# Kernel tuning notes

Hardware: AMD Instinct MI355X
Metric: run time of the kernel (lower is better)

Reference implementation:

```python
import jax, jax.numpy as jnp
import numpy as np

BATCH, SEQ, D_IN = 4, 2048, 1024
STATE, D_OUT, KX = 1024, 1024, 10


def setup_inputs() -> dict:
    key = jax.random.key(0)
    k0, k1, k2, k3, k4, k5 = jax.random.split(key, 6)
    inputs = jax.random.normal(k0, (BATCH, SEQ, D_IN), jnp.float32)
    h0 = jax.random.normal(k1, (STATE,), jnp.float32)
    A = jax.random.normal(k2, (STATE,), jnp.float32)
    A = A / jnp.max(jnp.abs(A))  # matches init_A / max|init_A|
    B = jax.random.normal(k3, (D_IN, STATE), jnp.float32) / D_IN
    C = jax.random.normal(k4, (STATE, D_OUT), jnp.float32) / STATE
    M = jax.random.normal(k5, (D_IN, D_OUT, KX), jnp.float32) / D_OUT
    return {"inputs": inputs, "h0": h0, "A": A, "B": B, "C": C, "M": M}


def compute_ar_x_preds(w, x):
    # w: (d_out, d_in, k); x: (b, l, d_in)
    d_out, d_in, k = w.shape
    b, l, _ = x.shape
    o = jnp.einsum('oik,bli->bklo', w, x)  # (b, k, l, d_out)
    shifts = jnp.arange(k)
    # roll slice i forward by i along the length axis
    o = jax.vmap(lambda oi, s: jnp.roll(oi, s, axis=1), in_axes=(1, 0), out_axes=1)(o, shifts)
    # triu mask: keep position t in slice i only if t >= i (causal AR)
    m = (jnp.arange(l)[None, :] >= shifts[:, None]).astype(o.dtype)  # (k, l)
    return jnp.sum(o * m[None, :, :, None], axis=1)  # (b, l, d_out)


def reference(inputs, h0, A, B, C, M):
    bsz = inputs.shape[0]
    h_init = jnp.broadcast_to(h0, (bsz, h0.shape[0]))  # h0.expand(bsz, state_dim)
    u_seq = jnp.swapaxes(inputs, 0, 1)  # (l, b, d_in)

    def step(h, u):
        h_new = A * h + u @ B  # diagonal recurrence
        return h_new, h_new

    _, hs = jax.lax.scan(step, h_init, u_seq)  # (l, b, state)
    all_h_t = jnp.swapaxes(hs, 0, 1)  # (b, l, state)
    lds_out = all_h_t @ C  # (b, l, d_out)
    ar = compute_ar_x_preds(M, inputs)
    return lds_out + ar
```

## Files before the change

kernel.cpp:

```cpp
#include <hip/hip_runtime.h>
#include <stdint.h>

typedef unsigned short u16;
typedef __attribute__((ext_vector_type(4))) float f32x4;
typedef __attribute__((ext_vector_type(8))) short s16x8;

#define BATCH 4
#define SEQ   2048
#define DIM   1024
#define KX    10
#define PAD   16
#define SEQP  (SEQ+PAD)

__device__ __forceinline__ u16 f2b(float f) {
    union { float f; uint32_t u; } v; v.f = f;
    uint32_t u = v.u + 0x7fffu + ((v.u >> 16) & 1u);
    return (u16)(u >> 16);
}
__device__ __forceinline__ float b2f(u16 h) {
    union { uint32_t u; float f; } v; v.u = ((uint32_t)h) << 16;
    return v.f;
}

__device__ __forceinline__ void llds16(const u16* g, u16* l) {
    __builtin_amdgcn_global_load_lds(
        (const __attribute__((address_space(1))) uint32_t*)g,
        (__attribute__((address_space(3))) uint32_t*)l, 16, 0, 0);
}

#define PREP_X_END  8256
#define PREP_C_END  10304
#define PREP_M_END  14400

__global__ __launch_bounds__(256) void k_prep(
    const float* __restrict__ x, const float* __restrict__ B,
    const float* __restrict__ C, const float* __restrict__ M,
    u16* __restrict__ Xpad, u16* __restrict__ Btr, u16* __restrict__ Wall)
{
    __shared__ float tile[32][33];
    const int bid = blockIdx.x, tid = threadIdx.x;

    if (bid < PREP_X_END) {
        int idx = bid * 256 + tid;
        long e = (long)idx * 4;
        int i = (int)(e & 1023);
        int row = (int)(e >> 10);
        int t = row % SEQP;
        int b = row / SEQP;
        ushort4 o;
        if (t < PAD) {
            o.x = 0; o.y = 0; o.z = 0; o.w = 0;
        } else {
            const float4 v = *(const float4*)(x + (((long)(b * SEQ + (t - PAD)) << 10) + i));
            o.x = f2b(v.x); o.y = f2b(v.y); o.z = f2b(v.z); o.w = f2b(v.w);
        }
        *(ushort4*)(Xpad + ((long)row << 10) + i) = o;
    } else if (bid < PREP_C_END) {
        const int tb = bid - PREP_X_END;
        const float* in = (tb < 1024) ? B : C;
        u16* out = (tb < 1024) ? Btr : Wall;
        int lb = tb & 1023;
        int bx = lb & 31, by = lb >> 5;
        int tx = tid & 31, ty = tid >> 5;
#pragma unroll
        for (int j = 0; j < 4; j++)
            tile[ty + j * 8][tx] = in[(long)(by * 32 + ty + j * 8) * 1024 + bx * 32 + tx];
        __syncthreads();
#pragma unroll
        for (int j = 0; j < 4; j++)
            out[(long)(bx * 32 + ty + j * 8) * 1024 + by * 32 + tx] = f2b(tile[tx][ty + j * 8]);
    } else {
        int idx = (bid - PREP_C_END) * 256 + tid;
        int o = idx >> 10, i = idx & 1023;
        const float* src = M + (long)idx * KX;
#pragma unroll
        for (int k = 0; k < KX; k++)
            Wall[((long)(k + 1) << 20) + ((long)o << 10) + i] = f2b(src[k]);
    }
}


__global__ void k_scan1(const u16* __restrict__ U, const float* __restrict__ A,
                        float* __restrict__ F) {
    int s = blockIdx.x * 256 + threadIdx.x;
    int bc = blockIdx.y;
    int b = bc >> 4, c = bc & 15;
    float a = A[s];
    const u16* u = U + (((long)(b * SEQ + c * 128)) << 10) + s;
    float f = 0.f;
#pragma unroll 8
    for (int j = 0; j < 128; j++) f = fmaf(a, f, b2f(u[(long)j << 10]));
    F[((long)bc << 10) + s] = f;
}

__global__ void k_scan2(const float* __restrict__ F, const float* __restrict__ A,
                        const float* __restrict__ h0, float* __restrict__ Carry) {
    int idx = blockIdx.x * 256 + threadIdx.x;
    int b = idx >> 10, s = idx & 1023;
    float a = A[s];
    float a128 = a;
#pragma unroll
    for (int q = 0; q < 7; q++) a128 *= a128;
    float carry = h0[s];
#pragma unroll
    for (int c = 0; c < 16; c++) {
        long off = ((long)(b * 16 + c) << 10) + s;
        Carry[off] = carry;
        carry = fmaf(a128, carry, F[off]);
    }
}

__global__ void k_scan3(u16* __restrict__ U, const float* __restrict__ A,
                        const float* __restrict__ Carry) {
    int s = blockIdx.x * 256 + threadIdx.x;
    int bc = blockIdx.y;
    int b = bc >> 4, c = bc & 15;
    float a = A[s];
    long base = (((long)(b * SEQ + c * 128)) << 10) + s;
    float h = Carry[((long)bc << 10) + s];
#pragma unroll 8
    for (int j = 0; j < 128; j++) {
        h = fmaf(a, h, b2f(U[base + ((long)j << 10)]));
        U[base + ((long)j << 10)] = f2b(h);
    }
}

__global__ __launch_bounds__(256) void k_gemm(
    void* __restrict__ outv, const u16* __restrict__ Xpad,
    const u16* __restrict__ Hbf, const u16* __restrict__ W,
    int ngroups, int use_h, int bf16_out)
{
    __shared__ u16 Asl[160 * 64];
    __shared__ u16 Wb2[2][128 * 64];

    const int tid  = threadIdx.x;
    const int wave = tid >> 6, lane = tid & 63;
    const int wm = wave >> 1, wn = wave & 1;
    const int quad = lane >> 4, l15 = lane & 15, l7 = lane & 7;

    const int col0 = blockIdx.x * 128;
    const int row0 = blockIdx.y * 128;
    const int bb = row0 >> 11;
    const long Xrow0 = (long)bb * SEQP + PAD + (row0 & (SEQ - 1));
    const long XslabBase = (Xrow0 - 16) << 10;
    const int lastg = ngroups - 1;

    f32x4 acc[4][4];
#pragma unroll
    for (int i = 0; i < 4; i++)
#pragma unroll
        for (int j = 0; j < 4; j++)
            acc[i][j] = (f32x4){0.f, 0.f, 0.f, 0.f};

    for (int k0 = 0; k0 < 1024; k0 += 64) {
#pragma unroll
        for (int q = 0; q < 5; q++) {
            int u = wave * 320 + q * 64 + lane;
            int row = u >> 3;
            int kc = (u & 7) ^ (row & 7);
            llds16(Xpad + XslabBase + ((long)row << 10) + k0 + kc * 8,
                   &Asl[(wave * 320 + q * 64) * 8]);
        }
        {
            int wsel = use_h ? 1 : 0;
            const u16* Wg = W + ((long)wsel << 20) + ((long)col0 << 10);
#pragma unroll
            for (int q = 0; q < 4; q++) {
                int u = wave * 256 + q * 64 + lane;
                int row = u >> 3;
                int kc = (u & 7) ^ (row & 7);
                llds16(Wg + ((long)row << 10) + k0 + kc * 8,
                       &Wb2[0][(wave * 256 + q * 64) * 8]);
            }
        }
        __syncthreads();

        for (int g = 0; g < ngroups; g++) {
            const bool isH = use_h && (g == lastg);
            if (isH) {
                const u16* Hb = Hbf + ((long)row0 << 10);
#pragma unroll
                for (int q = 0; q < 4; q++) {
                    int u = wave * 256 + q * 64 + lane;
                    int row = u >> 3;
                    int kc = (u & 7) ^ (row & 7);
                    llds16(Hb + ((long)row << 10) + k0 + kc * 8,
                           &Asl[(wave * 256 + q * 64) * 8]);
                }
                __syncthreads();
            }
            if (g < lastg) {
                int gn = g + 1;
                int wsel = use_h ? ((gn == lastg) ? 0 : gn + 1) : gn;
                const u16* Wg = W + ((long)wsel << 20) + ((long)col0 << 10);
                u16* dst = Wb2[gn & 1];
#pragma unroll
                for (int q = 0; q < 4; q++) {
                    int u = wave * 256 + q * 64 + lane;
                    int row = u >> 3;
                    int kc = (u & 7) ^ (row & 7);
                    llds16(Wg + ((long)row << 10) + k0 + kc * 8,
                           &dst[(wave * 256 + q * 64) * 8]);
                }
            }

            const int rbase = isH ? 0 : (16 - g);
            const int r7 = (l15 + rbase) & 7;
            const u16* Wrd = Wb2[g & 1];

            s16x8 af[4][2], bfr[4][2];
#pragma unroll
            for (int mi = 0; mi < 4; mi++) {
                int arow = rbase + wm * 64 + mi * 16 + l15;
#pragma unroll
                for (int kk = 0; kk < 2; kk++) {
                    int kca = ((kk * 4 + quad) ^ r7) << 3;
                    int kcb = ((kk * 4 + quad) ^ l7) << 3;
                    af[mi][kk]  = *(const s16x8*)&Asl[arow * 64 + kca];
                    bfr[mi][kk] = *(const s16x8*)&Wrd[(wn * 64 + mi * 16 + l15) * 64 + kcb];
                }
            }
#pragma unroll
            for (int mi = 0; mi < 4; mi++)
#pragma unroll
                for (int ni = 0; ni < 4; ni++) {
                    acc[mi][ni] = __builtin_amdgcn_mfma_f32_16x16x32_bf16(
                        af[mi][0], bfr[ni][0], acc[mi][ni], 0, 0, 0);
                    acc[mi][ni] = __builtin_amdgcn_mfma_f32_16x16x32_bf16(
                        af[mi][1], bfr[ni][1], acc[mi][ni], 0, 0, 0);
                }
            __syncthreads();
        }
    }

#pragma unroll
    for (int mi = 0; mi < 4; mi++) {
        int r = row0 + wm * 64 + mi * 16 + quad * 4;
#pragma unroll
        for (int ni = 0; ni < 4; ni++) {
            int c = col0 + wn * 64 + ni * 16 + l15;
            f32x4 v = acc[mi][ni];
            if (bf16_out) {
                u16* ob = (u16*)outv;
#pragma unroll
                for (int reg = 0; reg < 4; reg++)
                    ob[((long)(r + reg) << 10) + c] = f2b(v[reg]);
            } else {
                float* of = (float*)outv;
#pragma unroll
                for (int reg = 0; reg < 4; reg++)
                    of[((long)(r + reg) << 10) + c] = v[reg];
            }
        }
    }
}


extern "C" void kernel_launch(void* const* d_in, const int* in_sizes, int n_in,
                              void* d_out, int out_size, void* d_ws, size_t ws_size,
                              hipStream_t stream) {
    const float* x  = (const float*)d_in[0];
    const float* h0 = (const float*)d_in[1];
    const float* A  = (const float*)d_in[2];
    const float* B  = (const float*)d_in[3];
    const float* C  = (const float*)d_in[4];
    const float* M  = (const float*)d_in[5];
    float* out = (float*)d_out;

    char* ws = (char*)d_ws;
    u16*   Xpad  = (u16*)  (ws);
    u16*   Wall  = (u16*)  (ws + 16908288);
    u16*   Btr   = (u16*)  (ws + 39976960);
    u16*   Ubf   = (u16*)  (ws + 42074112);
    float* F     = (float*)(ws + 58851328);
    float* Carry = (float*)(ws + 59113472);

    k_prep<<<dim3(PREP_M_END), dim3(256), 0, stream>>>(x, B, C, M, Xpad, Btr, Wall);

    k_gemm<<<dim3(8, 64), dim3(256), 0, stream>>>(Ubf, Xpad, Ubf, Btr, 1, 0, 1);

    k_scan1<<<dim3(4, 64), dim3(256), 0, stream>>>(Ubf, A, F);
    k_scan2<<<dim3(16), dim3(256), 0, stream>>>(F, A, h0, Carry);
    k_scan3<<<dim3(4, 64), dim3(256), 0, stream>>>(Ubf, A, Carry);

    k_gemm<<<dim3(8, 64), dim3(256), 0, stream>>>(out, Xpad, Ubf, Wall, 11, 1, 0);
}
```

Before: 337.0 us.

## Load GEMM weight fragments directly into registers and template the kernel

The weight tile no longer goes through LDS. Each wave loads its B fragments straight from global memory into registers, double-buffered across the groups. The H slab gets its own LDS buffer loaded up front, which removes the per-group __syncthreads barriers and the mid-loop H reload. The kernel is templated on group count and flags so the group loop fully unrolls, it asks for 2 blocks per CU via launch bounds, and the grid is flattened to 1D. The cost is uncoalesced 16-byte global loads of W per lane and higher register pressure.

```diff
diff --git a/kernel.cpp b/kernel.cpp
--- a/kernel.cpp
+++ b/kernel.cpp
@@ -125,25 +125,25 @@
     }
 }
 
-__global__ __launch_bounds__(256) void k_gemm(
+template<int NG, int USE_H, int BF16_OUT>
+__global__ __launch_bounds__(256, 2) void k_gemm(
     void* __restrict__ outv, const u16* __restrict__ Xpad,
-    const u16* __restrict__ Hbf, const u16* __restrict__ W,
-    int ngroups, int use_h, int bf16_out)
+    const u16* __restrict__ Hbf, const u16* __restrict__ W)
 {
     __shared__ u16 Asl[160 * 64];
-    __shared__ u16 Wb2[2][128 * 64];
+    __shared__ u16 Hsl[(USE_H ? 128 : 1) * 64];
 
     const int tid  = threadIdx.x;
     const int wave = tid >> 6, lane = tid & 63;
     const int wm = wave >> 1, wn = wave & 1;
-    const int quad = lane >> 4, l15 = lane & 15, l7 = lane & 7;
-
-    const int col0 = blockIdx.x * 128;
-    const int row0 = blockIdx.y * 128;
+    const int quad = lane >> 4, l15 = lane & 15;
+
+    const int bid  = blockIdx.x;
+    const int col0 = (bid & 7) * 128;
+    const int row0 = (bid >> 3) * 128;
     const int bb = row0 >> 11;
     const long Xrow0 = (long)bb * SEQP + PAD + (row0 & (SEQ - 1));
     const long XslabBase = (Xrow0 - 16) << 10;
-    const int lastg = ngroups - 1;
 
     f32x4 acc[4][4];
 #pragma unroll
@@ -151,6 +151,8 @@
 #pragma unroll
         for (int j = 0; j < 4; j++)
             acc[i][j] = (f32x4){0.f, 0.f, 0.f, 0.f};
+
+    s16x8 bfrag[2][8];
 
     for (int k0 = 0; k0 < 1024; k0 += 64) {
 #pragma unroll
@@ -161,63 +163,55 @@
             llds16(Xpad + XslabBase + ((long)row << 10) + k0 + kc * 8,
                    &Asl[(wave * 320 + q * 64) * 8]);
         }
-        {
-            int wsel = use_h ? 1 : 0;
-            const u16* Wg = W + ((long)wsel << 20) + ((long)col0 << 10);
+        if (USE_H) {
+            const u16* Hb = Hbf + ((long)row0 << 10);
 #pragma unroll
             for (int q = 0; q < 4; q++) {
                 int u = wave * 256 + q * 64 + lane;
                 int row = u >> 3;
                 int kc = (u & 7) ^ (row & 7);
-                llds16(Wg + ((long)row << 10) + k0 + kc * 8,
-                       &Wb2[0][(wave * 256 + q * 64) * 8]);
-            }
+                llds16(Hb + ((long)row << 10) + k0 + kc * 8,
+                       &Hsl[(wave * 256 + q * 64) * 8]);
+            }
+        }
+        {
+            const int wsel0 = USE_H ? 1 : 0;
+            const u16* wp = W + ((long)wsel0 << 20) + ((long)(col0 + wn * 64) << 10) + k0;
+#pragma unroll
+            for (int ni = 0; ni < 4; ni++)
+#pragma unroll
+                for (int kk = 0; kk < 2; kk++)
+                    bfrag[0][ni * 2 + kk] =
+                        *(const s16x8*)(wp + ((l15 + ni * 16) << 10) + kk * 32 + quad * 8);
         }
         __syncthreads();
 
-        for (int g = 0; g < ngroups; g++) {
-            const bool isH = use_h && (g == lastg);
-            if (isH) {
-                const u16* Hb = Hbf + ((long)row0 << 10);
-#pragma unroll
-                for (int q = 0; q < 4; q++) {
-                    int u = wave * 256 + q * 64 + lane;
-                    int row = u >> 3;
-                    int kc = (u & 7) ^ (row & 7);
-                    llds16(Hb + ((long)row << 10) + k0 + kc * 8,
-                           &Asl[(wave * 256 + q * 64) * 8]);
-                }
-                __syncthreads();
-            }
-            if (g < lastg) {
-                int gn = g + 1;
-                int wsel = use_h ? ((gn == lastg) ? 0 : gn + 1) : gn;
-                const u16* Wg = W + ((long)wsel << 20) + ((long)col0 << 10);
-                u16* dst = Wb2[gn & 1];
-#pragma unroll
-                for (int q = 0; q < 4; q++) {
-                    int u = wave * 256 + q * 64 + lane;
-                    int row = u >> 3;
-                    int kc = (u & 7) ^ (row & 7);
-                    llds16(Wg + ((long)row << 10) + k0 + kc * 8,
-                           &dst[(wave * 256 + q * 64) * 8]);
-                }
-            }
-
+#pragma unroll
+        for (int g = 0; g < NG; g++) {
+            if (g + 1 < NG) {
+                const int wsel = USE_H ? ((g + 1 == NG - 1) ? 0 : g + 2) : g + 1;
+                const u16* wp = W + ((long)wsel << 20) + ((long)(col0 + wn * 64) << 10) + k0;
+#pragma unroll
+                for (int ni = 0; ni < 4; ni++)
+#pragma unroll
+                    for (int kk = 0; kk < 2; kk++)
+                        bfrag[(g + 1) & 1][ni * 2 + kk] =
+                            *(const s16x8*)(wp + ((l15 + ni * 16) << 10) + kk * 32 + quad * 8);
+            }
+
+            const bool isH = USE_H && (g == NG - 1);
+            const u16* abase = isH ? Hsl : Asl;
             const int rbase = isH ? 0 : (16 - g);
             const int r7 = (l15 + rbase) & 7;
-            const u16* Wrd = Wb2[g & 1];
-
-            s16x8 af[4][2], bfr[4][2];
+
+            s16x8 af[4][2];
 #pragma unroll
             for (int mi = 0; mi < 4; mi++) {
                 int arow = rbase + wm * 64 + mi * 16 + l15;
 #pragma unroll
                 for (int kk = 0; kk < 2; kk++) {
                     int kca = ((kk * 4 + quad) ^ r7) << 3;
-                    int kcb = ((kk * 4 + quad) ^ l7) << 3;
-                    af[mi][kk]  = *(const s16x8*)&Asl[arow * 64 + kca];
-                    bfr[mi][kk] = *(const s16x8*)&Wrd[(wn * 64 + mi * 16 + l15) * 64 + kcb];
+                    af[mi][kk] = *(const s16x8*)&abase[arow * 64 + kca];
                 }
             }
 #pragma unroll
@@ -225,12 +219,12 @@
 #pragma unroll
                 for (int ni = 0; ni < 4; ni++) {
                     acc[mi][ni] = __builtin_amdgcn_mfma_f32_16x16x32_bf16(
-                        af[mi][0], bfr[ni][0], acc[mi][ni], 0, 0, 0);
+                        af[mi][0], bfrag[g & 1][ni * 2 + 0], acc[mi][ni], 0, 0, 0);
                     acc[mi][ni] = __builtin_amdgcn_mfma_f32_16x16x32_bf16(
-                        af[mi][1], bfr[ni][1], acc[mi][ni], 0, 0, 0);
+                        af[mi][1], bfrag[g & 1][ni * 2 + 1], acc[mi][ni], 0, 0, 0);
                 }
-            __syncthreads();
-        }
+        }
+        __syncthreads();
     }
 
 #pragma unroll
@@ -240,7 +234,7 @@
         for (int ni = 0; ni < 4; ni++) {
             int c = col0 + wn * 64 + ni * 16 + l15;
             f32x4 v = acc[mi][ni];
-            if (bf16_out) {
+            if (BF16_OUT) {
                 u16* ob = (u16*)outv;
 #pragma unroll
                 for (int reg = 0; reg < 4; reg++)
@@ -277,11 +271,11 @@
 
     k_prep<<<dim3(PREP_M_END), dim3(256), 0, stream>>>(x, B, C, M, Xpad, Btr, Wall);
 
-    k_gemm<<<dim3(8, 64), dim3(256), 0, stream>>>(Ubf, Xpad, Ubf, Btr, 1, 0, 1);
+    k_gemm<1, 0, 1><<<dim3(512), dim3(256), 0, stream>>>(Ubf, Xpad, Ubf, Btr);
 
     k_scan1<<<dim3(4, 64), dim3(256), 0, stream>>>(Ubf, A, F);
     k_scan2<<<dim3(16), dim3(256), 0, stream>>>(F, A, h0, Carry);
     k_scan3<<<dim3(4, 64), dim3(256), 0, stream>>>(Ubf, A, Carry);
 
-    k_gemm<<<dim3(8, 64), dim3(256), 0, stream>>>(out, Xpad, Ubf, Wall, 11, 1, 0);
-}
+    k_gemm<11, 1, 0><<<dim3(512), dim3(256), 0, stream>>>(out, Xpad, Ubf, Wall);
+}
```

Result: slower. 510.0 us (+51.3%).

## Enlarge GEMM tiles to 256 rows, template kernel, split-K with atomics for output

Applied to the files above, without the earlier changes.

The GEMM kernel is templated on group count, H usage, output type and K-split, and compiled with unrolled group loops. Each block now runs 512 threads over a 256x128 tile, so each weight tile loaded into LDS is reused across twice as many rows. The final output GEMM splits K in two and accumulates into a zeroed output with float atomics, restoring grid parallelism after the larger tiles. This costs an extra memset, atomic traffic, nondeterministic summation order, higher LDS use per block, and shifted workspace offsets to pad the larger input slab.

```diff
diff --git a/kernel.cpp b/kernel.cpp
--- a/kernel.cpp
+++ b/kernel.cpp
@@ -125,25 +125,29 @@
     }
 }
 
-__global__ __launch_bounds__(256) void k_gemm(
+template<int NG, int USE_H, int BF16_OUT, int KSPLIT>
+__global__ __launch_bounds__(512, 4) void k_gemm(
     void* __restrict__ outv, const u16* __restrict__ Xpad,
-    const u16* __restrict__ Hbf, const u16* __restrict__ W,
-    int ngroups, int use_h, int bf16_out)
+    const u16* __restrict__ Hbf, const u16* __restrict__ W)
 {
-    __shared__ u16 Asl[160 * 64];
+    __shared__ u16 Asl[320 * 64];
     __shared__ u16 Wb2[2][128 * 64];
 
     const int tid  = threadIdx.x;
     const int wave = tid >> 6, lane = tid & 63;
     const int wm = wave >> 1, wn = wave & 1;
-    const int quad = lane >> 4, l15 = lane & 15, l7 = lane & 7;
-
-    const int col0 = blockIdx.x * 128;
-    const int row0 = blockIdx.y * 128;
+    const int quad = lane >> 4, l15 = lane & 15;
+
+    const int bid  = blockIdx.x;
+    const int col0 = (bid & 7) * 128;
+    const int row0 = ((bid >> 3) & 31) * 256;
+    const int kh   = (KSPLIT > 1) ? (bid >> 8) : 0;
+    const int kbeg = kh * (1024 / KSPLIT);
+    const int kend = kbeg + (1024 / KSPLIT);
+
     const int bb = row0 >> 11;
     const long Xrow0 = (long)bb * SEQP + PAD + (row0 & (SEQ - 1));
     const long XslabBase = (Xrow0 - 16) << 10;
-    const int lastg = ngroups - 1;
 
     f32x4 acc[4][4];
 #pragma unroll
@@ -152,7 +156,7 @@
         for (int j = 0; j < 4; j++)
             acc[i][j] = (f32x4){0.f, 0.f, 0.f, 0.f};
 
-    for (int k0 = 0; k0 < 1024; k0 += 64) {
+    for (int k0 = kbeg; k0 < kend; k0 += 64) {
 #pragma unroll
         for (int q = 0; q < 5; q++) {
             int u = wave * 320 + q * 64 + lane;
@@ -162,21 +166,22 @@
                    &Asl[(wave * 320 + q * 64) * 8]);
         }
         {
-            int wsel = use_h ? 1 : 0;
-            const u16* Wg = W + ((long)wsel << 20) + ((long)col0 << 10);
-#pragma unroll
-            for (int q = 0; q < 4; q++) {
-                int u = wave * 256 + q * 64 + lane;
+            const int wsel0 = USE_H ? 1 : 0;
+            const u16* Wg = W + ((long)wsel0 << 20) + ((long)col0 << 10);
+#pragma unroll
+            for (int q = 0; q < 2; q++) {
+                int u = wave * 128 + q * 64 + lane;
                 int row = u >> 3;
                 int kc = (u & 7) ^ (row & 7);
                 llds16(Wg + ((long)row << 10) + k0 + kc * 8,
-                       &Wb2[0][(wave * 256 + q * 64) * 8]);
+                       &Wb2[0][(wave * 128 + q * 64) * 8]);
             }
         }
         __syncthreads();
 
-        for (int g = 0; g < ngroups; g++) {
-            const bool isH = use_h && (g == lastg);
+#pragma unroll
+        for (int g = 0; g < NG; g++) {
+            const bool isH = USE_H && (g == NG - 1);
             if (isH) {
                 const u16* Hb = Hbf + ((long)row0 << 10);
 #pragma unroll
@@ -189,18 +194,17 @@
                 }
                 __syncthreads();
             }
-            if (g < lastg) {
-                int gn = g + 1;
-                int wsel = use_h ? ((gn == lastg) ? 0 : gn + 1) : gn;
+            if (g + 1 < NG) {
+                const int wsel = USE_H ? ((g + 1 == NG - 1) ? 0 : g + 2) : g + 1;
                 const u16* Wg = W + ((long)wsel << 20) + ((long)col0 << 10);
-                u16* dst = Wb2[gn & 1];
-#pragma unroll
-                for (int q = 0; q < 4; q++) {
-                    int u = wave * 256 + q * 64 + lane;
+                u16* dst = Wb2[(g + 1) & 1];
+#pragma unroll
+                for (int q = 0; q < 2; q++) {
+                    int u = wave * 128 + q * 64 + lane;
                     int row = u >> 3;
                     int kc = (u & 7) ^ (row & 7);
                     llds16(Wg + ((long)row << 10) + k0 + kc * 8,
-                           &dst[(wave * 256 + q * 64) * 8]);
+                           &dst[(wave * 128 + q * 64) * 8]);
                 }
             }
 
@@ -215,7 +219,7 @@
 #pragma unroll
                 for (int kk = 0; kk < 2; kk++) {
                     int kca = ((kk * 4 + quad) ^ r7) << 3;
-                    int kcb = ((kk * 4 + quad) ^ l7) << 3;
+                    int kcb = ((kk * 4 + quad) ^ (l15 & 7)) << 3;
                     af[mi][kk]  = *(const s16x8*)&Asl[arow * 64 + kca];
                     bfr[mi][kk] = *(const s16x8*)&Wrd[(wn * 64 + mi * 16 + l15) * 64 + kcb];
                 }
@@ -240,11 +244,17 @@
         for (int ni = 0; ni < 4; ni++) {
             int c = col0 + wn * 64 + ni * 16 + l15;
             f32x4 v = acc[mi][ni];
-            if (bf16_out) {
+            if (BF16_OUT) {
                 u16* ob = (u16*)outv;
 #pragma unroll
                 for (int reg = 0; reg < 4; reg++)
                     ob[((long)(r + reg) << 10) + c] = f2b(v[reg]);
+            } else if (KSPLIT > 1) {
+                float* of = (float*)outv;
+#pragma unroll
+                for (int reg = 0; reg < 4; reg++)
+                    __hip_atomic_fetch_add(of + (((long)(r + reg) << 10) + c), v[reg],
+                                           __ATOMIC_RELAXED, __HIP_MEMORY_SCOPE_AGENT);
             } else {
                 float* of = (float*)outv;
 #pragma unroll
@@ -269,19 +279,20 @@
 
     char* ws = (char*)d_ws;
     u16*   Xpad  = (u16*)  (ws);
-    u16*   Wall  = (u16*)  (ws + 16908288);
-    u16*   Btr   = (u16*)  (ws + 39976960);
-    u16*   Ubf   = (u16*)  (ws + 42074112);
-    float* F     = (float*)(ws + 58851328);
-    float* Carry = (float*)(ws + 59113472);
+    u16*   Wall  = (u16*)  (ws + 17006592);
+    u16*   Btr   = (u16*)  (ws + 40075264);
+    u16*   Ubf   = (u16*)  (ws + 42172416);
+    float* F     = (float*)(ws + 58949632);
+    float* Carry = (float*)(ws + 59211776);
 
     k_prep<<<dim3(PREP_M_END), dim3(256), 0, stream>>>(x, B, C, M, Xpad, Btr, Wall);
 
-    k_gemm<<<dim3(8, 64), dim3(256), 0, stream>>>(Ubf, Xpad, Ubf, Btr, 1, 0, 1);
+    k_gemm<1, 0, 1, 1><<<dim3(256), dim3(512), 0, stream>>>(Ubf, Xpad, Ubf, Btr);
 
     k_scan1<<<dim3(4, 64), dim3(256), 0, stream>>>(Ubf, A, F);
     k_scan2<<<dim3(16), dim3(256), 0, stream>>>(F, A, h0, Carry);
     k_scan3<<<dim3(4, 64), dim3(256), 0, stream>>>(Ubf, A, Carry);
 
-    k_gemm<<<dim3(8, 64), dim3(256), 0, stream>>>(out, Xpad, Ubf, Wall, 11, 1, 0);
-}
+    hipMemsetAsync(d_out, 0, (size_t)out_size * sizeof(float), stream);
+    k_gemm<11, 1, 0, 2><<<dim3(512), dim3(512), 0, stream>>>(out, Xpad, Ubf, Wall);
+}
```

New measurement: 392.1 us. +16.3%, slower.
